# Optimization experiments

Hardware: AMD Instinct MI355X
Metric: run time of the kernel (lower is better)

The kernel has to match this reference:

```python
import jax, jax.numpy as jnp
import numpy as np

NZ = 128
N_GEN = 8
BATCH = 2048
SLOPE = 0.2


def _convt(x, w, b, stride, pad):
    # PyTorch ConvTranspose2d(weight [Cin,Cout,kH,kW], stride, padding p)
    # == conv with lhs_dilation=stride, padding=k-1-p, spatially-flipped
    # kernel with in/out channels swapped.
    k = jnp.flip(w, axis=(2, 3)).transpose(2, 3, 0, 1)  # [kH,kW,Cin,Cout]
    y = jax.lax.conv_general_dilated(
        x, k, window_strides=(1, 1), padding=[(pad, pad), (pad, pad)],
        lhs_dilation=(stride, stride),
        dimension_numbers=('NCHW', 'HWIO', 'NCHW'))
    return y + b[None, :, None, None]


def setup_inputs() -> dict:
    key = jax.random.key(0)
    ks = jax.random.split(key, 12)
    s = 0.05
    return {
        'z': jax.random.normal(ks[0], (BATCH, NZ), jnp.float32),
        'g_idx': jax.random.randint(ks[1], (BATCH,), 0, N_GEN),
        'W1': jax.random.normal(ks[2], (N_GEN, NZ, 256), jnp.float32) * s,
        'b1': jax.random.normal(ks[3], (N_GEN, 256), jnp.float32) * s,
        'W2': jax.random.normal(ks[4], (N_GEN, 256, 1568), jnp.float32) * s,
        'b2': jax.random.normal(ks[5], (N_GEN, 1568), jnp.float32) * s,
        'cw1': jax.random.normal(ks[6], (N_GEN, 32, 16, 4, 4), jnp.float32) * s,
        'cb1': jax.random.normal(ks[7], (N_GEN, 16), jnp.float32) * s,
        'cw2': jax.random.normal(ks[8], (N_GEN, 16, 8, 4, 4), jnp.float32) * s,
        'cb2': jax.random.normal(ks[9], (N_GEN, 8), jnp.float32) * s,
        'cw3': jax.random.normal(ks[10], (N_GEN, 8, 1, 3, 3), jnp.float32) * s,
        'cb3': jax.random.normal(ks[11], (N_GEN, 1), jnp.float32) * s,
    }


def _single_gen(params, z):
    W1, b1, W2, b2, cw1, cb1, cw2, cb2, cw3, cb3 = params
    lrelu = lambda x: jax.nn.leaky_relu(x, SLOPE)
    h = lrelu(z @ W1 + b1)                 # [B,256]
    h = lrelu(h @ W2 + b2)                 # [B,1568]
    h = h.reshape(-1, 32, 7, 7)
    h = lrelu(_convt(h, cw1, cb1, 2, 2))   # [B,16,14,14]
    h = lrelu(_convt(h, cw2, cb2, 2, 2))   # [B,8,28,28]
    return jnp.tanh(_convt(h, cw3, cb3, 1, 1))  # [B,1,28,28]


def reference(z, g_idx, W1, b1, W2, b2, cw1, cb1, cw2, cb2, cw3, cb3):
    params = (W1, b1, W2, b2, cw1, cb1, cw2, cb2, cw3, cb3)
    # Compute every generator on the full batch (faithful to the torch loop),
    # vmapped over the generator axis: images [G,B,1,28,28].
    images = jax.vmap(_single_gen, in_axes=((0,) * 10, None))(params, z)
    # Per-sample gather: keep generator g_idx[b] for each sample b.
    return images[g_idx, jnp.arange(z.shape[0])]
```

## Files before the change

### kernel.cpp

```cpp
#include <hip/hip_runtime.h>
#include <cstdint>
#include <cstddef>

#define BATCH 2048
#define NZ 128
#define NGEN 8
#define GRPS 32
#define MAXG 72
#define NCT 13
#define H2_ELEMS 1792
#define WS_H1_OFF 16384
#define WS_H2_OFF (16384 + MAXG * 8192 * 4)
#define WS_W2T_OFF (WS_H2_OFF + BATCH * H2_ELEMS * 2)
#define W2T_GSTRIDE (1568 * 256)
#define NB_W2T (NGEN * 49)
#define NB_PREP (NB_W2T + MAXG * 4)
#define WS_WPK1_OFF (WS_W2T_OFF + NGEN * W2T_GSTRIDE * 2)
#define WS_WPK2_OFF (WS_WPK1_OFF + NGEN * 4096 * 4)
#define WS_WPK3_OFF (WS_WPK2_OFF + NGEN * 1024 * 4)
#define PS 168

typedef unsigned int u32;
typedef unsigned short u16;
typedef unsigned long long u64;
typedef _Float16 f16x8 __attribute__((ext_vector_type(8)));
typedef _Float16 f16x4 __attribute__((ext_vector_type(4)));
typedef _Float16 f16x2 __attribute__((ext_vector_type(2)));
typedef float f32x4 __attribute__((ext_vector_type(4)));

__device__ __forceinline__ float lrelu(float x) { return fmaxf(x, 0.2f * x); }
__device__ __forceinline__ u16 f16b(float f) {
    _Float16 h = (_Float16)f;
    return __builtin_bit_cast(u16, h);
}
__device__ __forceinline__ u32 pk2(float a, float b) {
    f16x2 v; v[0] = (_Float16)a; v[1] = (_Float16)b;
    return __builtin_bit_cast(u32, v);
}
__device__ __forceinline__ float dot2(u32 a, u32 b, float c) {
#if __has_builtin(__builtin_amdgcn_fdot2)
    return __builtin_amdgcn_fdot2(__builtin_bit_cast(f16x2, a),
                                  __builtin_bit_cast(f16x2, b), c, false);
#else
    float d;
    asm("v_dot2_f32_f16 %0, %1, %2, %3" : "=v"(d) : "v"(a), "v"(b), "v"(c));
    return d;
#endif
}
__device__ __forceinline__ float fast_tanh(float x) {
    x = fminf(fmaxf(x, -9.f), 9.f);
    const float e = __expf(2.f * x);
    return (e - 1.f) / (e + 1.f);
}
__device__ __forceinline__ int h2off(int n) {
    const int ci = n / 49, rm = n % 49;
    return ci * 56 + (rm / 7) * 8 + (rm % 7);
}

__global__ __launch_bounds__(256) void prep_kernel(
    const float* __restrict__ z, const int* __restrict__ g_idx,
    const float* __restrict__ W1, const float* __restrict__ b1,
    const float* __restrict__ W2, int* __restrict__ wsi,
    float* __restrict__ h1g, _Float16* __restrict__ W2T,
    const float* __restrict__ cw1, const float* __restrict__ cw2,
    const float* __restrict__ cw3,
    u32* __restrict__ wpk1, u32* __restrict__ wpk2, u32* __restrict__ wpk3)
{
    __shared__ __align__(16) char pmem[16896];

    const int tid = threadIdx.x;
    const int bx = blockIdx.x;

    if (bx < NB_W2T) {
        _Float16 (*t)[264] = (_Float16 (*)[264])pmem;
        const int g = bx / 49;
        const int n0 = (bx % 49) * 32;
        const float* src = W2 + (size_t)g * 256 * 1568;
        const int nl = tid & 31, kh = tid >> 5;
        #pragma unroll 8
        for (int p = 0; p < 32; ++p) {
            const int k = p * 8 + kh;
            t[nl][k] = (_Float16)src[(size_t)k * 1568 + n0 + nl];
        }
        __syncthreads();
        _Float16* dst = W2T + (size_t)g * W2T_GSTRIDE + (size_t)n0 * 256;
        #pragma unroll
        for (int ii = 0; ii < 4; ++ii) {
            const int i = tid + 256 * ii;
            const int n = i >> 5, kc = i & 31;
            *(uint4*)(dst + (size_t)n * 256 + kc * 8) = *(const uint4*)&t[n][kc * 8];
        }
        return;
    }

    if (bx >= NB_PREP && bx < NB_PREP + NGEN) {
        const int g = bx - NB_PREP;
        const float* c1p = cw1 + g * 8192;
        u32* o1 = wpk1 + g * 4096;
        for (int i = tid; i < 4096; i += 256) {
            const int cip = i >> 8, a = (i >> 6) & 3, co = (i >> 2) & 15, c = i & 3;
            const float* s = c1p + cip * 512 + co * 16 + a * 4 + c;
            o1[i] = pk2(s[0], s[256]);
        }
        const float* c2p = cw2 + g * 2048;
        u32* o2 = wpk2 + g * 1024;
        for (int i = tid; i < 1024; i += 256) {
            const int cip = i >> 7, a = (i >> 5) & 3, co = (i >> 2) & 7, c = i & 3;
            const float* s = c2p + cip * 256 + co * 16 + a * 4 + c;
            o2[i] = pk2(s[0], s[128]);
        }
        if (tid < 36) {
            const int cip = tid / 9, r = tid % 9;
            const float* s = cw3 + g * 72 + cip * 18 + r;
            wpk3[g * 36 + tid] = pk2(s[0], s[9]);
        }
        return;
    }

    u16* rank       = (u16*)pmem;
    int (*wcnt)[NGEN]  = (int (*)[NGEN])(pmem + 4096);
    int (*wboff)[NGEN] = (int (*)[NGEN])(pmem + 4224);
    int* pbase      = (int*)(pmem + 4352);
    const int w = tid >> 6, lane = tid & 63;
    if (tid < 4 * NGEN) wcnt[tid >> 3][tid & 7] = 0;
    __syncthreads();
    const u64 lt = ((u64)1 << lane) - 1;
    #pragma unroll
    for (int r = 0; r < 8; ++r) {
        const int b = r * 256 + tid;
        const int gg = g_idx[b];
        u64 m[NGEN];
        #pragma unroll
        for (int k = 0; k < NGEN; ++k) m[k] = __ballot(gg == k);
        rank[b] = (u16)((int)__popcll(m[gg] & lt) + wcnt[w][gg]);
        if (lane < NGEN) wcnt[w][lane] += (int)__popcll(m[lane]);
    }
    __syncthreads();
    if (tid == 0) {
        int acc = 0;
        for (int g = 0; g < NGEN; ++g) {
            pbase[g] = acc;
            const int tot = wcnt[0][g] + wcnt[1][g] + wcnt[2][g] + wcnt[3][g];
            acc += ((tot + GRPS - 1) / GRPS) * GRPS;
        }
        pbase[NGEN] = acc;
    }
    __syncthreads();
    if (tid < 32) {
        const int ww = tid >> 3, g = tid & 7;
        int off = pbase[g];
        for (int w2 = 0; w2 < ww; ++w2) off += wcnt[w2][g];
        wboff[ww][g] = off;
    }
    __syncthreads();

    if (bx >= NB_PREP + NGEN) {
        if (tid == 0) wsi[0] = pbase[NGEN];
        for (int i = tid; i < MAXG * GRPS; i += 256) wsi[16 + i] = -1;
        __syncthreads();
        #pragma unroll
        for (int r = 0; r < 8; ++r) {
            const int b = r * 256 + tid;
            const int gg = g_idx[b];
            wsi[16 + wboff[w][gg] + (int)rank[b]] = b;
        }
        return;
    }

    const int bx2 = bx - NB_W2T;
    const int grp = bx2 >> 2;
    const int s0 = (bx2 & 3) * 8;
    if (grp * GRPS >= pbase[NGEN]) return;

    int gsel = 0;
    #pragma unroll
    for (int g = 1; g < NGEN; ++g) if (grp * GRPS >= pbase[g]) gsel = g;

    int* sb = (int*)(pmem + 4400);
    float (*zst)[12] = (float (*)[12])(pmem + 4608);
    if (tid < 8) sb[tid] = -1;
    __syncthreads();
    const int base = grp * GRPS + s0;
    #pragma unroll
    for (int r = 0; r < 8; ++r) {
        const int b = r * 256 + tid;
        const int gg = g_idx[b];
        const int rel = wboff[w][gg] + (int)rank[b] - base;
        if ((unsigned)rel < 8u) sb[rel] = b;
    }
    __syncthreads();

    const float* W1g = W1 + gsel * (NZ * 256);
    const float* b1g = b1 + gsel * 256;

    {
        const int s = tid >> 5, f = tid & 31;
        float4 v = make_float4(0.f, 0.f, 0.f, 0.f);
        if (sb[s] >= 0) v = *(const float4*)(z + (size_t)sb[s] * NZ + 4 * f);
        zst[4 * f + 0][s] = v.x; zst[4 * f + 1][s] = v.y;
        zst[4 * f + 2][s] = v.z; zst[4 * f + 3][s] = v.w;
    }
    __syncthreads();

    const int c = tid;
    float acc[8];
    #pragma unroll
    for (int s = 0; s < 8; ++s) acc[s] = 0.f;
    const float* wp = W1g + c;
    #pragma unroll 4
    for (int k = 0; k < NZ; ++k) {
        const float wv = wp[k * 256];
        float av[8];
        *(float4*)&av[0] = *(const float4*)&zst[k][0];
        *(float4*)&av[4] = *(const float4*)&zst[k][4];
        #pragma unroll
        for (int s = 0; s < 8; ++s) acc[s] += av[s] * wv;
    }
    const float bv = b1g[c];
    float* hp = h1g + (size_t)grp * 8192 + (size_t)s0 * 256 + c;
    #pragma unroll
    for (int s = 0; s < 8; ++s) hp[s * 256] = lrelu(acc[s] + bv);
}

__global__ __launch_bounds__(256) void fc2_kernel(
    const int* __restrict__ g_idx,
    const _Float16* __restrict__ W2T, const float* __restrict__ b2,
    const int* __restrict__ wsi, const float* __restrict__ h1g,
    u16* __restrict__ h2g)
{
    __shared__ __align__(16) char afsm[16384];
    _Float16* afrag = (_Float16*)afsm;
    __shared__ int sb[GRPS];
    __shared__ int sG;

    const int tid = threadIdx.x;
    const int grp = blockIdx.x / NCT;
    const int tile = blockIdx.x % NCT;
    if (grp * GRPS >= wsi[0]) return;

    if (tid == 0) sG = g_idx[wsi[16 + grp * GRPS]];
    if (tid < GRPS) sb[tid] = wsi[16 + grp * GRPS + tid];
    __syncthreads();
    const _Float16* W2Tg = W2T + (size_t)sG * W2T_GSTRIDE;
    const float* b2g = b2 + sG * 1568;

    {
        const float4* h1p4 = (const float4*)(h1g + (size_t)grp * 8192);
        #pragma unroll
        for (int i = 0; i < 8; ++i) {
            const int u = tid + 256 * i;
            const int j4 = u & 1;
            const int ln = (u >> 1) & 63;
            const int kq = (u >> 7) & 7;
            const int mt = (u >> 10) & 1;
            const int s = mt * 16 + (ln & 15);
            const float4 v = h1p4[s * 64 + kq * 8 + ((ln >> 4) << 1) + j4];
            f16x4 hi;
            hi[0] = (_Float16)v.x; hi[1] = (_Float16)v.y;
            hi[2] = (_Float16)v.z; hi[3] = (_Float16)v.w;
            const int bh = ((mt * 8 + kq) * 64 + ln) * 8 + 4 * j4;
            *(f16x4*)&afrag[bh] = hi;
        }
    }
    __syncthreads();

    const int wave = tid >> 6;
    const int lane = tid & 63;
    const int q = lane >> 4;
    const int nl = lane & 15;
    const int nb0 = tile * 128 + 2 * wave * 16;
    const int nb1 = nb0 + 16;
    const bool act0 = nb0 < 1568, act1 = nb1 < 1568;

    f32x4 accA0 = {0.f, 0.f, 0.f, 0.f}, accB0 = accA0;
    f32x4 accA1 = accA0, accB1 = accA0;
    if (act0) {
        const _Float16* bp = W2Tg + (size_t)(nb0 + nl) * 256 + q * 8;
        #pragma unroll
        for (int kq = 0; kq < 8; ++kq) {
            const f16x8 b = *(const f16x8*)(bp + kq * 32);
            const f16x8 a0 = *(const f16x8*)&afrag[((0 * 8 + kq) * 64 + lane) * 8];
            const f16x8 a1 = *(const f16x8*)&afrag[((1 * 8 + kq) * 64 + lane) * 8];
            accA0 = __builtin_amdgcn_mfma_f32_16x16x32_f16(a0, b, accA0, 0, 0, 0);
            accB0 = __builtin_amdgcn_mfma_f32_16x16x32_f16(a1, b, accB0, 0, 0, 0);
        }
    }
    if (act1) {
        const _Float16* bp = W2Tg + (size_t)(nb1 + nl) * 256 + q * 8;
        #pragma unroll
        for (int kq = 0; kq < 8; ++kq) {
            const f16x8 b = *(const f16x8*)(bp + kq * 32);
            const f16x8 a0 = *(const f16x8*)&afrag[((0 * 8 + kq) * 64 + lane) * 8];
            const f16x8 a1 = *(const f16x8*)&afrag[((1 * 8 + kq) * 64 + lane) * 8];
            accA1 = __builtin_amdgcn_mfma_f32_16x16x32_f16(a0, b, accA1, 0, 0, 0);
            accB1 = __builtin_amdgcn_mfma_f32_16x16x32_f16(a1, b, accB1, 0, 0, 0);
        }
    }
    __syncthreads();

    u16* pst = (u16*)afsm;
    const int nstart = tile * 128;
    const int nend = (nstart + 128 < 1568) ? nstart + 128 : 1568;
    const int offLo = h2off(nstart), offHi = h2off(nend - 1);
    const int lo8 = offLo & ~7;

    if (act0) {
        const int n = nb0 + nl;
        const float bias = b2g[n];
        u16* pp = pst + (h2off(n) - lo8);
        #pragma unroll
        for (int reg = 0; reg < 4; ++reg) {
            pp[(q * 4 + reg) * PS]        = f16b(lrelu(accA0[reg] + bias));
            pp[(16 + q * 4 + reg) * PS]   = f16b(lrelu(accB0[reg] + bias));
        }
    }
    if (act1) {
        const int n = nb1 + nl;
        const float bias = b2g[n];
        u16* pp = pst + (h2off(n) - lo8);
        #pragma unroll
        for (int reg = 0; reg < 4; ++reg) {
            pp[(q * 4 + reg) * PS]        = f16b(lrelu(accA1[reg] + bias));
            pp[(16 + q * 4 + reg) * PS]   = f16b(lrelu(accB1[reg] + bias));
        }
    }
    __syncthreads();

    {
        const int s = tid >> 3, p = tid & 7;
        const int bb = sb[s];
        if (bb >= 0) {
            u16* row = h2g + (size_t)bb * H2_ELEMS;
            const u16* ps = pst + s * PS - lo8;
            const int c0 = (offLo + 7) & ~7;
            const int c1 = (offHi + 1) & ~7;
            for (int o = offLo + p; o < c0 && o <= offHi; o += 8) row[o] = ps[o];
            const int t0 = (c1 > offLo) ? c1 : offLo;
            for (int o = t0 + p; o <= offHi; o += 8) row[o] = ps[o];
            for (int c = c0 + p * 8; c + 8 <= c1; c += 64)
                *(uint4*)(row + c) = *(const uint4*)(ps + c);
        }
    }
}

__device__ __forceinline__ void conv2p_full(
    const u32 (*c1s)[14][20], u16* dst,
    const u32* __restrict__ w2g, const float bv, const int co, const int y)
{
    float acc[28];
    #pragma unroll
    for (int x = 0; x < 28; ++x) acc[x] = bv;
    const int a0 = (y + 1) & 1;
    for (int aa = 0; aa < 2; ++aa) {
        const int a = a0 + 2 * aa;
        const int iy = (y + 1 - a) >> 1;
        if ((unsigned)iy < 14u) {
            #pragma unroll 2
            for (int cip = 0; cip < 8; ++cip) {
                u32 rr[14];
                *(uint4*)&rr[0]  = *(const uint4*)&c1s[cip][iy][0];
                *(uint4*)&rr[4]  = *(const uint4*)&c1s[cip][iy][4];
                *(uint4*)&rr[8]  = *(const uint4*)&c1s[cip][iy][8];
                *(uint2*)&rr[12] = *(const uint2*)&c1s[cip][iy][12];
                const uint4 wq = *(const uint4*)(w2g + ((cip * 4 + a) * 8 + co) * 4);
                const u32 wv[4] = {wq.x, wq.y, wq.z, wq.w};
                #pragma unroll
                for (int x = 0; x < 28; ++x) {
                    const int c0v = (x + 1) & 1;
                    const int ix0 = (x + 1 - c0v) >> 1;
                    if (ix0 < 14) acc[x] = dot2(rr[ix0],     wv[c0v],     acc[x]);
                    if (ix0 >= 1) acc[x] = dot2(rr[ix0 - 1], wv[c0v + 2], acc[x]);
                }
            }
        }
    }
    #pragma unroll
    for (int x = 0; x < 28; ++x) dst[2 * (1 + x)] = f16b(lrelu(acc[x]));
}

__global__ __launch_bounds__(256, 6) void conv_kernel(
    const int* __restrict__ g_idx, const int* __restrict__ wsi,
    const u32* __restrict__ wpk1, const float* __restrict__ cb1,
    const u32* __restrict__ wpk2, const float* __restrict__ cb2,
    const u32* __restrict__ wpk3, const float* __restrict__ cb3,
    const u16* __restrict__ h2g, float* __restrict__ out)
{
    __shared__ __align__(16) char smem[8960 + 13440];
    u32 (*c1s)[14][20] = (u32 (*)[14][20])smem;
    u32 (*h2s)[7][8]   = (u32 (*)[7][8])(smem + 8960);
    u32 (*c2s)[28][30] = (u32 (*)[28][30])(smem + 8960);
    __shared__ u32 w3s[36];

    const int tid = threadIdx.x;
    const int b = wsi[16 + blockIdx.x];
    if (b < 0) return;
    const int g = g_idx[b];
    const u32* w1g = wpk1 + g * 4096;
    const u32* w2g = wpk2 + g * 1024;
    const float* cb1g = cb1 + g * 16;
    const float* cb2g = cb2 + g * 8;
    const float  cb3v = cb3[g];

    if (tid < 224) {
        const uint4 qv = ((const uint4*)(h2g + (size_t)b * H2_ELEMS))[tid];
        const int ci = tid / 7, yq = tid % 7;
        u16* dst = (u16*)&h2s[ci >> 1][yq][0] + (ci & 1);
        const u32 w[4] = {qv.x, qv.y, qv.z, qv.w};
        #pragma unroll
        for (int j = 0; j < 4; ++j) {
            dst[4 * j]     = (u16)(w[j] & 0xffffu);
            dst[4 * j + 2] = (u16)(w[j] >> 16);
        }
    }
    if (tid < 36) w3s[tid] = wpk3[g * 36 + tid];
    __syncthreads();

    if (tid < 224) {
        const int co = tid / 14, y = tid % 14;
        const float bv = cb1g[co];
        float acc[14];
        #pragma unroll
        for (int x = 0; x < 14; ++x) acc[x] = bv;
        const int a0 = (y + 1) & 1;
        for (int aa = 0; aa < 2; ++aa) {
            const int a = a0 + 2 * aa;
            const int iy = (y + 1 - a) >> 1;
            if ((unsigned)iy < 7u) {
                #pragma unroll 2
                for (int cip = 0; cip < 16; ++cip) {
                    u32 rr[8];
                    *(uint4*)&rr[0] = *(const uint4*)&h2s[cip][iy][0];
                    *(uint4*)&rr[4] = *(const uint4*)&h2s[cip][iy][4];
                    const uint4 wq = *(const uint4*)(w1g + ((cip * 4 + a) * 16 + co) * 4);
                    const u32 wv[4] = {wq.x, wq.y, wq.z, wq.w};
                    #pragma unroll
                    for (int x = 0; x < 14; ++x) {
                        const int c0v = (x + 1) & 1;
                        const int ix0 = (x + 1 - c0v) >> 1;
                        if (ix0 < 7)  acc[x] = dot2(rr[ix0],     wv[c0v],     acc[x]);
                        if (ix0 >= 1) acc[x] = dot2(rr[ix0 - 1], wv[c0v + 2], acc[x]);
                    }
                }
            }
        }
        u16* dst = (u16*)&c1s[co >> 1][y][0] + (co & 1);
        #pragma unroll
        for (int x = 0; x < 14; ++x) dst[2 * x] = f16b(lrelu(acc[x]));
    }
    __syncthreads();

    if (tid < 224) {
        const int zc = tid / 56, zr = tid % 56;
        c2s[zc][zr % 28][(zr < 28) ? 0 : 29] = 0u;
        const int co = tid / 28, y = tid % 28;
        const float bv = cb2g[co];
        u16* dst = (u16*)&c2s[co >> 1][y][0] + (co & 1);
        conv2p_full(c1s, dst, w2g, bv, co, y);
    }
    __syncthreads();

    if (tid < 196) {
        const int y = tid / 7, qq = tid % 7;
        const int xb = qq * 4;
        float acc[4] = {cb3v, cb3v, cb3v, cb3v};
        #pragma unroll 2
        for (int cip = 0; cip < 4; ++cip) {
            u32 wp[9];
            #pragma unroll
            for (int j = 0; j < 9; ++j) wp[j] = w3s[cip * 9 + j];
            #pragma unroll
            for (int a = 0; a < 3; ++a) {
                const int iy = y + 1 - a;
                if ((unsigned)iy < 28u) {
                    u32 rr[6];
                    *(uint2*)&rr[0] = *(const uint2*)&c2s[cip][iy][xb];
                    *(uint2*)&rr[2] = *(const uint2*)&c2s[cip][iy][xb + 2];
                    *(uint2*)&rr[4] = *(const uint2*)&c2s[cip][iy][xb + 4];
                    #pragma unroll
                    for (int xx = 0; xx < 4; ++xx)
                        #pragma unroll
                        for (int c = 0; c < 3; ++c)
                            acc[xx] = dot2(rr[xx + 2 - c], wp[a * 3 + c], acc[xx]);
                }
            }
        }
        float* op = out + (size_t)b * 784 + y * 28 + xb;
        #pragma unroll
        for (int xx = 0; xx < 4; ++xx) op[xx] = fast_tanh(acc[xx]);
    }
}

extern "C" void kernel_launch(void* const* d_in, const int* in_sizes, int n_in,
                              void* d_out, int out_size, void* d_ws, size_t ws_size,
                              hipStream_t stream) {
    const float* z   = (const float*)d_in[0];
    const int*   gi  = (const int*)d_in[1];
    const float* W1  = (const float*)d_in[2];
    const float* b1  = (const float*)d_in[3];
    const float* W2  = (const float*)d_in[4];
    const float* b2  = (const float*)d_in[5];
    const float* cw1 = (const float*)d_in[6];
    const float* cb1 = (const float*)d_in[7];
    const float* cw2 = (const float*)d_in[8];
    const float* cb2 = (const float*)d_in[9];
    const float* cw3 = (const float*)d_in[10];
    const float* cb3 = (const float*)d_in[11];
    int*      wsi = (int*)d_ws;
    float*    h1g = (float*)((char*)d_ws + WS_H1_OFF);
    u16*      h2g = (u16*)((char*)d_ws + WS_H2_OFF);
    _Float16* w2t = (_Float16*)((char*)d_ws + WS_W2T_OFF);
    u32*      wpk1 = (u32*)((char*)d_ws + WS_WPK1_OFF);
    u32*      wpk2 = (u32*)((char*)d_ws + WS_WPK2_OFF);
    u32*      wpk3 = (u32*)((char*)d_ws + WS_WPK3_OFF);

    prep_kernel<<<NB_PREP + NGEN + 1, 256, 0, stream>>>(z, gi, W1, b1, W2, wsi,
                                                        h1g, w2t, cw1, cw2, cw3,
                                                        wpk1, wpk2, wpk3);
    fc2_kernel<<<MAXG * NCT, 256, 0, stream>>>(gi, w2t, b2, wsi, h1g, h2g);
    conv_kernel<<<MAXG * GRPS, 256, 0, stream>>>(gi, wsi, wpk1, cb1, wpk2, cb2,
                                                 wpk3, cb3, h2g, (float*)d_out);
}
```

Baseline: 162.5 us.

## Widen fc2 column tile to 256 outputs per block, four MFMA tiles per wave

The fc2 kernel now gives each block 256 output columns instead of 128, so there are 7 column tiles rather than 13. Each wave computes four 16-column MFMA tiles and reuses the A fragments staged in shared memory across them. The shared staging buffer and its row pitch grow to fit the wider tile. The aim is to cut redundant h1 staging and block launch overhead, at the cost of fewer blocks, more accumulator registers per wave and more LDS per block, which may reduce occupancy.

```diff
diff --git a/kernel.cpp b/kernel.cpp
--- a/kernel.cpp
+++ b/kernel.cpp
@@ -7,7 +7,7 @@
 #define NGEN 8
 #define GRPS 32
 #define MAXG 72
-#define NCT 13
+#define NCT 7
 #define H2_ELEMS 1792
 #define WS_H1_OFF 16384
 #define WS_H2_OFF (16384 + MAXG * 8192 * 4)
@@ -18,7 +18,7 @@
 #define WS_WPK1_OFF (WS_W2T_OFF + NGEN * W2T_GSTRIDE * 2)
 #define WS_WPK2_OFF (WS_WPK1_OFF + NGEN * 4096 * 4)
 #define WS_WPK3_OFF (WS_WPK2_OFF + NGEN * 1024 * 4)
-#define PS 168
+#define PS 304
 
 typedef unsigned int u32;
 typedef unsigned short u16;
@@ -228,7 +228,7 @@
     const int* __restrict__ wsi, const float* __restrict__ h1g,
     u16* __restrict__ h2g)
 {
-    __shared__ __align__(16) char afsm[16384];
+    __shared__ __align__(16) char afsm[GRPS * PS * 2];
     _Float16* afrag = (_Float16*)afsm;
     __shared__ int sb[GRPS];
     __shared__ int sG;
@@ -268,60 +268,49 @@
     const int lane = tid & 63;
     const int q = lane >> 4;
     const int nl = lane & 15;
-    const int nb0 = tile * 128 + 2 * wave * 16;
-    const int nb1 = nb0 + 16;
-    const bool act0 = nb0 < 1568, act1 = nb1 < 1568;
-
-    f32x4 accA0 = {0.f, 0.f, 0.f, 0.f}, accB0 = accA0;
-    f32x4 accA1 = accA0, accB1 = accA0;
-    if (act0) {
-        const _Float16* bp = W2Tg + (size_t)(nb0 + nl) * 256 + q * 8;
-        #pragma unroll
-        for (int kq = 0; kq < 8; ++kq) {
-            const f16x8 b = *(const f16x8*)(bp + kq * 32);
-            const f16x8 a0 = *(const f16x8*)&afrag[((0 * 8 + kq) * 64 + lane) * 8];
-            const f16x8 a1 = *(const f16x8*)&afrag[((1 * 8 + kq) * 64 + lane) * 8];
-            accA0 = __builtin_amdgcn_mfma_f32_16x16x32_f16(a0, b, accA0, 0, 0, 0);
-            accB0 = __builtin_amdgcn_mfma_f32_16x16x32_f16(a1, b, accB0, 0, 0, 0);
-        }
-    }
-    if (act1) {
-        const _Float16* bp = W2Tg + (size_t)(nb1 + nl) * 256 + q * 8;
-        #pragma unroll
-        for (int kq = 0; kq < 8; ++kq) {
-            const f16x8 b = *(const f16x8*)(bp + kq * 32);
-            const f16x8 a0 = *(const f16x8*)&afrag[((0 * 8 + kq) * 64 + lane) * 8];
-            const f16x8 a1 = *(const f16x8*)&afrag[((1 * 8 + kq) * 64 + lane) * 8];
-            accA1 = __builtin_amdgcn_mfma_f32_16x16x32_f16(a0, b, accA1, 0, 0, 0);
-            accB1 = __builtin_amdgcn_mfma_f32_16x16x32_f16(a1, b, accB1, 0, 0, 0);
+    const int nbw = tile * 256 + wave * 64;
+
+    f32x4 accA[4], accB[4];
+    #pragma unroll
+    for (int nt = 0; nt < 4; ++nt) {
+        accA[nt] = (f32x4){0.f, 0.f, 0.f, 0.f};
+        accB[nt] = accA[nt];
+    }
+    #pragma unroll
+    for (int nt = 0; nt < 4; ++nt) {
+        const int nb = nbw + nt * 16;
+        if (nb < 1568) {
+            const _Float16* bp = W2Tg + (size_t)(nb + nl) * 256 + q * 8;
+            #pragma unroll
+            for (int kq = 0; kq < 8; ++kq) {
+                const f16x8 b = *(const f16x8*)(bp + kq * 32);
+                const f16x8 a0 = *(const f16x8*)&afrag[((0 * 8 + kq) * 64 + lane) * 8];
+                const f16x8 a1 = *(const f16x8*)&afrag[((1 * 8 + kq) * 64 + lane) * 8];
+                accA[nt] = __builtin_amdgcn_mfma_f32_16x16x32_f16(a0, b, accA[nt], 0, 0, 0);
+                accB[nt] = __builtin_amdgcn_mfma_f32_16x16x32_f16(a1, b, accB[nt], 0, 0, 0);
+            }
         }
     }
     __syncthreads();
 
     u16* pst = (u16*)afsm;
-    const int nstart = tile * 128;
-    const int nend = (nstart + 128 < 1568) ? nstart + 128 : 1568;
+    const int nstart = tile * 256;
+    const int nend = (nstart + 256 < 1568) ? nstart + 256 : 1568;
     const int offLo = h2off(nstart), offHi = h2off(nend - 1);
     const int lo8 = offLo & ~7;
 
-    if (act0) {
-        const int n = nb0 + nl;
-        const float bias = b2g[n];
-        u16* pp = pst + (h2off(n) - lo8);
-        #pragma unroll
-        for (int reg = 0; reg < 4; ++reg) {
-            pp[(q * 4 + reg) * PS]        = f16b(lrelu(accA0[reg] + bias));
-            pp[(16 + q * 4 + reg) * PS]   = f16b(lrelu(accB0[reg] + bias));
-        }
-    }
-    if (act1) {
-        const int n = nb1 + nl;
-        const float bias = b2g[n];
-        u16* pp = pst + (h2off(n) - lo8);
-        #pragma unroll
-        for (int reg = 0; reg < 4; ++reg) {
-            pp[(q * 4 + reg) * PS]        = f16b(lrelu(accA1[reg] + bias));
-            pp[(16 + q * 4 + reg) * PS]   = f16b(lrelu(accB1[reg] + bias));
+    #pragma unroll
+    for (int nt = 0; nt < 4; ++nt) {
+        const int nb = nbw + nt * 16;
+        if (nb < 1568) {
+            const int n = nb + nl;
+            const float bias = b2g[n];
+            u16* pp = pst + (h2off(n) - lo8);
+            #pragma unroll
+            for (int reg = 0; reg < 4; ++reg) {
+                pp[(q * 4 + reg) * PS]      = f16b(lrelu(accA[nt][reg] + bias));
+                pp[(16 + q * 4 + reg) * PS] = f16b(lrelu(accB[nt][reg] + bias));
+            }
         }
     }
     __syncthreads();
```

Measured after the change: 160.6 us. Within noise of the previous version (-1.2%).
